# Kernel optimization log

Measured on AMD Instinct MI355X. Metric: run time of the kernel, lower is better.

Reference implementation:

```python
import jax, jax.numpy as jnp
import numpy as np

D_MODEL = 1024
H = 16
D_HEAD = 64  # d_q = d_k = d_v
B = 2
S = 2048


def setup_inputs() -> dict:
    key = jax.random.key(0)
    ks = jax.random.split(key, 12)
    scale = 1.0 / np.sqrt(D_MODEL)
    inp = {
        "q": jax.random.normal(ks[0], (B, S, D_MODEL), dtype=jnp.float32),
        "k": jax.random.normal(ks[1], (B, S, D_MODEL), dtype=jnp.float32),
        "v": jax.random.normal(ks[2], (B, S, D_MODEL), dtype=jnp.float32),
        "mask": jax.random.uniform(ks[3], (S, S), dtype=jnp.float32),
        # stacked per-head projection weights: [H, d_model, d_head]
        "W_q": jax.random.normal(ks[4], (H, D_MODEL, D_HEAD), dtype=jnp.float32) * scale,
        "b_q": jnp.zeros((H, D_HEAD), dtype=jnp.float32),
        "W_k": jax.random.normal(ks[5], (H, D_MODEL, D_HEAD), dtype=jnp.float32) * scale,
        "b_k": jnp.zeros((H, D_HEAD), dtype=jnp.float32),
        "W_v": jax.random.normal(ks[6], (H, D_MODEL, D_HEAD), dtype=jnp.float32) * scale,
        "b_v": jnp.zeros((H, D_HEAD), dtype=jnp.float32),
        # output projection: [H*d_v, d_model]
        "W_o": jax.random.normal(ks[7], (H * D_HEAD, D_MODEL), dtype=jnp.float32) * (1.0 / np.sqrt(H * D_HEAD)),
        "b_o": jnp.zeros((D_MODEL,), dtype=jnp.float32),
    }
    return inp


def reference(q, k, v, mask, W_q, b_q, W_k, b_k, W_v, b_v, W_o, b_o):
    # Batched QKV projections over all heads (original loops per head).
    Q = jnp.einsum("bsd,hde->bhse", q, W_q) + b_q[None, :, None, :]  # [B,H,S,Dh]
    K = jnp.einsum("bsd,hde->bhse", k, W_k) + b_k[None, :, None, :]
    V = jnp.einsum("bsd,hde->bhse", v, W_v) + b_v[None, :, None, :]
    scale = 1.0 / jnp.sqrt(jnp.asarray(D_HEAD, dtype=Q.dtype))
    # NOTE: mask is MULTIPLICATIVE on the scaled scores (as in the original).
    scores = jnp.einsum("bhse,bhte->bhst", Q, K) * scale * mask  # [B,H,S,S]
    attn = jax.nn.softmax(scores, axis=-1)
    heads = jnp.einsum("bhst,bhte->bhse", attn, V)  # [B,H,S,Dh]
    # concat heads along feature dim (head order matches torch cat order)
    concat = jnp.transpose(heads, (0, 2, 1, 3)).reshape(B, S, H * D_HEAD)
    return concat @ W_o + b_o
```

## Files before the change

### kernel.cpp

```cpp
#include <hip/hip_runtime.h>
#include <stdint.h>

#define DM 1024
#define HNUM 16
#define DH 64
#define BB 2
#define SSEQ 2048

typedef unsigned short ushort_t;
typedef __attribute__((ext_vector_type(8))) short bf16x8;
typedef __attribute__((ext_vector_type(4))) float f32x4;
typedef __attribute__((ext_vector_type(16))) float f32x16;

#define SCALE2 0.18033688011112042f
#define DEFER_THR 11.0f

__device__ __forceinline__ ushort_t f2bf(float f) {
  unsigned u = __builtin_bit_cast(unsigned, f);
  u += 0x7FFFu + ((u >> 16) & 1u);
  return (ushort_t)(u >> 16);
}
__device__ __forceinline__ float bf2f(ushort_t h) {
  return __builtin_bit_cast(float, (unsigned)h << 16);
}
__device__ __forceinline__ float fast_exp2(float x) {
#if __has_builtin(__builtin_amdgcn_exp2f)
  return __builtin_amdgcn_exp2f(x);
#else
  return exp2f(x);
#endif
}
__device__ __forceinline__ unsigned cvt_pk_bf16(float lo, float hi) {
  unsigned r;
  asm("v_cvt_pk_bf16_f32 %0, %1, %2" : "=v"(r) : "v"(lo), "v"(hi));
  return r;
}
__device__ __forceinline__ void plane32_swap(unsigned& a, unsigned& b, int hh) {
#if __has_builtin(__builtin_amdgcn_permlane32_swap)
  typedef int v2i __attribute__((ext_vector_type(2)));
  v2i r = __builtin_amdgcn_permlane32_swap((int)a, (int)b, 0, 0);
  a = (unsigned)r.x; b = (unsigned)r.y;
#else
  unsigned sa = (unsigned)__shfl_xor((int)a, 32);
  unsigned sb = (unsigned)__shfl_xor((int)b, 32);
  unsigned na = hh ? sb : a;
  unsigned nb = hh ? b : sa;
  a = na; b = nb;
#endif
}

typedef const __attribute__((address_space(1))) unsigned int* gas_ptr;
typedef __attribute__((address_space(3))) unsigned int* las_ptr;
__device__ __forceinline__ void gload_lds16(const void* g, void* l) {
  __builtin_amdgcn_global_load_lds((gas_ptr)(uintptr_t)g, (las_ptr)(uintptr_t)l, 16, 0, 0);
}

__global__ void cvt_f32_bf16(const float* __restrict__ src, ushort_t* __restrict__ dst, int n8) {
  int idx = blockIdx.x * 256 + threadIdx.x;
  if (idx >= n8) return;
  const float4* s4 = (const float4*)src;
  float4 a = s4[idx * 2], c = s4[idx * 2 + 1];
  union { ushort_t h[8]; uint4 u; } o;
  o.h[0] = f2bf(a.x); o.h[1] = f2bf(a.y); o.h[2] = f2bf(a.z); o.h[3] = f2bf(a.w);
  o.h[4] = f2bf(c.x); o.h[5] = f2bf(c.y); o.h[6] = f2bf(c.z); o.h[7] = f2bf(c.w);
  ((uint4*)dst)[idx] = o.u;
}

__global__ void mask_pack(const float* __restrict__ src, ushort_t* __restrict__ dst) {
  const int TG = blockIdx.x;
  const int T = TG >> 6, G = TG & 63;
  const int tid = threadIdx.x;
  #pragma unroll
  for (int i = 0; i < 2; ++i) {
    const int wd = tid * 2 + i;
    const int l = wd & 63, g2 = (wd >> 6) & 3, a = wd >> 8;
    const int q = G * 32 + (l & 31);
    const int t = T * 64 + a * 32 + g2 * 8 + (l >> 5) * 4;
    float4 mv = *(const float4*)(src + (size_t)q * 2048 + t);
    union { ushort_t h4[4]; uint2 u; } pk;
    pk.h4[0] = f2bf(mv.x * SCALE2); pk.h4[1] = f2bf(mv.y * SCALE2);
    pk.h4[2] = f2bf(mv.z * SCALE2); pk.h4[3] = f2bf(mv.w * SCALE2);
    *(uint2*)(dst + (size_t)TG * 2048 + (size_t)wd * 4) = pk.u;
  }
}

__global__ void transpose_cvt(const float* __restrict__ src, ushort_t* __restrict__ dst, int R, int C) {
  __shared__ ushort_t T[64][65];
  const int g = blockIdx.z;
  const int r0 = blockIdx.y * 64, c0 = blockIdx.x * 64;
  src += (size_t)g * R * C;
  dst += (size_t)g * R * C;
  const int tid = threadIdx.x;
  #pragma unroll
  for (int i = 0; i < 16; ++i) {
    int idx = i * 256 + tid;
    int r = idx >> 6, c = idx & 63;
    T[r][c] = f2bf(src[(size_t)(r0 + r) * C + c0 + c]);
  }
  __syncthreads();
  #pragma unroll
  for (int i = 0; i < 16; ++i) {
    int idx = i * 256 + tid;
    int cc = idx >> 6, rr = idx & 63;
    dst[(size_t)(c0 + cc) * R + r0 + rr] = T[rr][cc];
  }
}

__device__ __forceinline__ void gemm_mainloop_128(const ushort_t* __restrict__ A,
                                                  const ushort_t* __restrict__ Bm,
                                                  f32x4 (&acc)[4][4], int m0, int n0, int l, int w) {
  __shared__ ushort_t As[128 * 64];
  __shared__ ushort_t Bs[128 * 64];
  const int wr = w >> 1, wc = w & 1;
  for (int ks = 0; ks < 16; ++ks) {
    const int k0 = ks * 64;
    #pragma unroll
    for (int it = 0; it < 4; ++it) {
      const int chunk = it * 4 + w;
      const int row = chunk * 8 + (l >> 3);
      const int kc = ((l & 7) * 8) ^ ((row & 7) * 8);
      gload_lds16(A + (size_t)(m0 + row) * 1024 + k0 + kc, (char*)As + chunk * 1024);
      gload_lds16(Bm + (size_t)(n0 + row) * 1024 + k0 + kc, (char*)Bs + chunk * 1024);
    }
    __syncthreads();
    #pragma unroll
    for (int kk = 0; kk < 2; ++kk) {
      bf16x8 af[4], bfr[4];
      #pragma unroll
      for (int mi = 0; mi < 4; ++mi) {
        const int row = wr * 64 + mi * 16 + (l & 15);
        const int kc = (kk * 32 + (l >> 4) * 8) ^ ((row & 7) * 8);
        af[mi] = *(const bf16x8*)(As + row * 64 + kc);
      }
      #pragma unroll
      for (int ni = 0; ni < 4; ++ni) {
        const int row = wc * 64 + ni * 16 + (l & 15);
        const int kc = (kk * 32 + (l >> 4) * 8) ^ ((row & 7) * 8);
        bfr[ni] = *(const bf16x8*)(Bs + row * 64 + kc);
      }
      #pragma unroll
      for (int mi = 0; mi < 4; ++mi)
        #pragma unroll
        for (int ni = 0; ni < 4; ++ni)
          acc[mi][ni] = __builtin_amdgcn_mfma_f32_16x16x32_bf16(af[mi], bfr[ni], acc[mi][ni], 0, 0, 0);
    }
    __syncthreads();
  }
}

__global__ __launch_bounds__(256, 2) void qkv_gemm(
    const ushort_t* __restrict__ qb, const ushort_t* __restrict__ kb, const ushort_t* __restrict__ vb,
    const ushort_t* __restrict__ Wtq, const ushort_t* __restrict__ Wtk, const ushort_t* __restrict__ Wtv,
    const float* __restrict__ bq, const float* __restrict__ bk, const float* __restrict__ bv,
    ushort_t* __restrict__ Qo, ushort_t* __restrict__ Ko, ushort_t* __restrict__ Vto) {
  const int z = blockIdx.z;
  const ushort_t* A  = z == 0 ? qb : (z == 1 ? kb : vb);
  const ushort_t* Bm = z == 0 ? Wtq : (z == 1 ? Wtk : Wtv);
  const float* bias  = z == 0 ? bq : (z == 1 ? bk : bv);
  ushort_t* out      = z == 0 ? Qo : (z == 1 ? Ko : Vto);
  const int m0 = blockIdx.x * 128, n0 = blockIdx.y * 128;
  const int tid = threadIdx.x, l = tid & 63, w = tid >> 6;
  f32x4 acc[4][4] = {};
  gemm_mainloop_128(A, Bm, acc, m0, n0, l, w);
  const int wr = w >> 1, wc = w & 1;
  #pragma unroll
  for (int mi = 0; mi < 4; ++mi) {
    #pragma unroll
    for (int ni = 0; ni < 4; ++ni) {
      const int n = n0 + wc * 64 + ni * 16 + (l & 15);
      const float bb = bias[n];
      const int mbase = m0 + wr * 64 + mi * 16 + ((l >> 4) << 2);
      if (z < 2) {
        #pragma unroll
        for (int i = 0; i < 4; ++i) {
          const int m = mbase + i;
          const size_t o = (((size_t)((m >> 11) * 16 + (n >> 6))) * 2048 + (m & 2047)) * 64 + (n & 63);
          out[o] = f2bf(acc[mi][ni][i] + bb);
        }
      } else {
        union { ushort_t h[4]; uint2 u2; } pk;
        #pragma unroll
        for (int i = 0; i < 4; ++i) pk.h[i] = f2bf(acc[mi][ni][i] + bb);
        const size_t o = (((size_t)((mbase >> 11) * 16 + (n >> 6))) * 64 + (n & 63)) * 2048 + (mbase & 2047);
        *(uint2*)(out + o) = pk.u2;
      }
    }
  }
}

__global__ __launch_bounds__(256, 2) void out_gemm(const ushort_t* __restrict__ A,
                                                   const ushort_t* __restrict__ Bm,
                                                   const float* __restrict__ bias,
                                                   float* __restrict__ out) {
  const int m0 = blockIdx.x * 128, n0 = blockIdx.y * 128;
  const int tid = threadIdx.x, l = tid & 63, w = tid >> 6;
  f32x4 acc[4][4] = {};
  gemm_mainloop_128(A, Bm, acc, m0, n0, l, w);
  const int wr = w >> 1, wc = w & 1;
  #pragma unroll
  for (int mi = 0; mi < 4; ++mi) {
    #pragma unroll
    for (int ni = 0; ni < 4; ++ni) {
      const int n = n0 + wc * 64 + ni * 16 + (l & 15);
      const float bb = bias[n];
      const int mbase = m0 + wr * 64 + mi * 16 + ((l >> 4) << 2);
      #pragma unroll
      for (int i = 0; i < 4; ++i)
        out[(size_t)(mbase + i) * 1024 + n] = acc[mi][ni][i] + bb;
    }
  }
}

__device__ __forceinline__ void stage_kv(const ushort_t* __restrict__ Kb, const ushort_t* __restrict__ Vb,
                                         int t0, ushort_t* ks, ushort_t* vs, int l, int w) {
  #pragma unroll
  for (int half = 0; half < 2; ++half) {
    const int c = half * 4 + w;
    const int r1 = c * 8 + (l >> 3);
    const int cc = ((l & 7) * 8) ^ ((r1 & 7) * 8);
    gload_lds16(Kb + (size_t)(t0 + r1) * 64 + cc, (char*)ks + c * 1024);
    gload_lds16(Vb + (size_t)r1 * 2048 + t0 + cc, (char*)vs + c * 1024);
  }
}

__global__ __launch_bounds__(256, 2) void flash_attn(const ushort_t* __restrict__ Q,
                                                     const ushort_t* __restrict__ K,
                                                     const ushort_t* __restrict__ Vt,
                                                     const ushort_t* __restrict__ maskF,
                                                     ushort_t* __restrict__ concat) {
  const int bh = blockIdx.y, b = bh >> 4, h = bh & 15;
  const int tid = threadIdx.x, l = tid & 63, w = tid >> 6;
  const int hh = l >> 5, q_l = l & 31;
  __shared__ ushort_t Ks[2][64 * 64];
  __shared__ ushort_t Vs[2][64 * 64];
  const ushort_t* Qb = Q + (size_t)bh * 2048 * 64;
  const ushort_t* Kb = K + (size_t)bh * 2048 * 64;
  const ushort_t* Vb = Vt + (size_t)bh * 64 * 2048;
  const int qbase = blockIdx.x * 128 + w * 32;
  const int G = qbase >> 5;

  bf16x8 qf[4];
  #pragma unroll
  for (int s = 0; s < 4; ++s)
    qf[s] = *(const bf16x8*)(Qb + (size_t)(qbase + q_l) * 64 + s * 16 + hh * 8);

  float m_run = -1e30f, l_run = 0.f;
  f32x16 po[2] = {};

  stage_kv(Kb, Vb, 0, Ks[0], Vs[0], l, w);
  int cur = 0;

  for (int t0 = 0; t0 < 2048; t0 += 64) {
    __syncthreads();
    if (t0 + 64 < 2048) stage_kv(Kb, Vb, t0 + 64, Ks[cur ^ 1], Vs[cur ^ 1], l, w);

    const ushort_t* mbase = maskF + (size_t)((t0 >> 6) * 64 + G) * 2048;
    uint2 mw[2][4];
    #pragma unroll
    for (int a = 0; a < 2; ++a)
      #pragma unroll
      for (int g2 = 0; g2 < 4; ++g2)
        mw[a][g2] = *(const uint2*)(mbase + (size_t)(((a * 4 + g2) * 64) + l) * 4);

    f32x16 sc[2] = {};
    #pragma unroll
    for (int s = 0; s < 4; ++s) {
      #pragma unroll
      for (int mt = 0; mt < 2; ++mt) {
        const int row = mt * 32 + q_l;
        const int col = (s * 16 + hh * 8) ^ ((row & 7) * 8);
        const bf16x8 kf = *(const bf16x8*)(Ks[cur] + row * 64 + col);
        sc[mt] = __builtin_amdgcn_mfma_f32_32x32x16_bf16(kf, qf[s], sc[mt], 0, 0, 0);
      }
    }

    float tmax = -1e30f;
    #pragma unroll
    for (int a = 0; a < 2; ++a) {
      #pragma unroll
      for (int g2 = 0; g2 < 4; ++g2) {
        const unsigned lo = mw[a][g2].x, hi = mw[a][g2].y;
        float v0 = sc[a][g2 * 4 + 0] * bf2f((ushort_t)lo);
        float v1 = sc[a][g2 * 4 + 1] * bf2f((ushort_t)(lo >> 16));
        float v2 = sc[a][g2 * 4 + 2] * bf2f((ushort_t)hi);
        float v3 = sc[a][g2 * 4 + 3] * bf2f((ushort_t)(hi >> 16));
        sc[a][g2 * 4 + 0] = v0; sc[a][g2 * 4 + 1] = v1;
        sc[a][g2 * 4 + 2] = v2; sc[a][g2 * 4 + 3] = v3;
        tmax = fmaxf(tmax, fmaxf(fmaxf(v0, v1), fmaxf(v2, v3)));
      }
    }
    tmax = fmaxf(tmax, __shfl_xor(tmax, 32));

    if (!__all(tmax <= m_run + DEFER_THR)) {
      const float mnew = fmaxf(m_run, tmax);
      const float rf = fast_exp2(m_run - mnew);
      m_run = mnew;
      l_run *= rf;
      #pragma unroll
      for (int et = 0; et < 2; ++et)
        #pragma unroll
        for (int r = 0; r < 16; ++r) po[et][r] *= rf;
    }

    float psum = 0.f;
    unsigned pw[2][8];
    #pragma unroll
    for (int a = 0; a < 2; ++a)
      #pragma unroll
      for (int j = 0; j < 8; ++j) {
        const float p0 = fast_exp2(sc[a][2 * j] - m_run);
        const float p1 = fast_exp2(sc[a][2 * j + 1] - m_run);
        psum += p0 + p1;
        pw[a][j] = cvt_pk_bf16(p0, p1);
      }
    psum += __shfl_xor(psum, 32);
    l_run += psum;

    #pragma unroll
    for (int a = 0; a < 2; ++a) {
      plane32_swap(pw[a][0], pw[a][2], hh);
      plane32_swap(pw[a][1], pw[a][3], hh);
      plane32_swap(pw[a][4], pw[a][6], hh);
      plane32_swap(pw[a][5], pw[a][7], hh);
    }

    #pragma unroll
    for (int s = 0; s < 4; ++s) {
      union { unsigned u[4]; bf16x8 v; } pf;
      pf.u[0] = pw[s >> 1][(s & 1) * 4 + 0];
      pf.u[1] = pw[s >> 1][(s & 1) * 4 + 1];
      pf.u[2] = pw[s >> 1][(s & 1) * 4 + 2];
      pf.u[3] = pw[s >> 1][(s & 1) * 4 + 3];
      #pragma unroll
      for (int et = 0; et < 2; ++et) {
        const int row = et * 32 + q_l;
        const int col = (s * 16 + hh * 8) ^ ((row & 7) * 8);
        const bf16x8 vf = *(const bf16x8*)(Vs[cur] + row * 64 + col);
        po[et] = __builtin_amdgcn_mfma_f32_32x32x16_bf16(vf, pf.v, po[et], 0, 0, 0);
      }
    }
    cur ^= 1;
  }

  const float invl = 1.0f / l_run;
  __syncthreads();
  ushort_t* ow = &Ks[0][0] + w * 2048;
  #pragma unroll
  for (int et = 0; et < 2; ++et)
    #pragma unroll
    for (int r = 0; r < 16; ++r) {
      const int e = et * 32 + (r & 3) + 8 * (r >> 2) + 4 * hh;
      const int ba = (q_l * 128 + e * 2) ^ ((q_l & 7) << 4);
      *(ushort_t*)((char*)ow + ba) = f2bf(po[et][r] * invl);
    }
  __syncthreads();
  {
    union { ushort_t hs[32]; uint2 u2[8]; uint4 u4[4]; } ov;
    const int ebase = hh * 32;
    #pragma unroll
    for (int c = 0; c < 8; ++c) {
      const int e0 = ebase + c * 4;
      const int ba = (q_l * 128 + e0 * 2) ^ ((q_l & 7) << 4);
      ov.u2[c] = *(const uint2*)((const char*)ow + ba);
    }
    ushort_t* dst = concat + ((size_t)(b * 2048 + qbase + q_l)) * 1024 + h * 64 + ebase;
    #pragma unroll
    for (int c2 = 0; c2 < 4; ++c2)
      ((uint4*)dst)[c2] = ov.u4[c2];
  }
}

extern "C" void kernel_launch(void* const* d_in, const int* in_sizes, int n_in,
                              void* d_out, int out_size, void* d_ws, size_t ws_size,
                              hipStream_t stream) {
  const float* q    = (const float*)d_in[0];
  const float* k    = (const float*)d_in[1];
  const float* v    = (const float*)d_in[2];
  const float* mask = (const float*)d_in[3];
  const float* Wq   = (const float*)d_in[4];
  const float* bq   = (const float*)d_in[5];
  const float* Wk   = (const float*)d_in[6];
  const float* bk   = (const float*)d_in[7];
  const float* Wv   = (const float*)d_in[8];
  const float* bv   = (const float*)d_in[9];
  const float* Wo   = (const float*)d_in[10];
  const float* bo   = (const float*)d_in[11];

  const size_t SZ8M = (size_t)4096 * 1024 * 2;
  const size_t SZ2M = (size_t)1024 * 1024 * 2;
  if (ws_size < 7 * SZ8M + 4 * SZ2M) return;

  char* p = (char*)d_ws;
  ushort_t* qb    = (ushort_t*)p; p += SZ8M;
  ushort_t* kb    = (ushort_t*)p; p += SZ8M;
  ushort_t* vb    = (ushort_t*)p; p += SZ8M;
  ushort_t* maskb = (ushort_t*)p; p += SZ8M;
  ushort_t* Qo    = (ushort_t*)p; p += SZ8M;
  ushort_t* Ko    = (ushort_t*)p; p += SZ8M;
  ushort_t* Vto   = (ushort_t*)p; p += SZ8M;
  ushort_t* Wtq   = (ushort_t*)p; p += SZ2M;
  ushort_t* Wtk   = (ushort_t*)p; p += SZ2M;
  ushort_t* Wtv   = (ushort_t*)p; p += SZ2M;
  ushort_t* Wot   = (ushort_t*)p; p += SZ2M;
  ushort_t* concat = qb;

  const int n8 = (4096 * 1024) / 8;
  cvt_f32_bf16<<<dim3(2048), dim3(256), 0, stream>>>(q, qb, n8);
  cvt_f32_bf16<<<dim3(2048), dim3(256), 0, stream>>>(k, kb, n8);
  cvt_f32_bf16<<<dim3(2048), dim3(256), 0, stream>>>(v, vb, n8);
  mask_pack<<<dim3(2048), dim3(256), 0, stream>>>(mask, maskb);
  transpose_cvt<<<dim3(1, 16, 16), dim3(256), 0, stream>>>(Wq, Wtq, 1024, 64);
  transpose_cvt<<<dim3(1, 16, 16), dim3(256), 0, stream>>>(Wk, Wtk, 1024, 64);
  transpose_cvt<<<dim3(1, 16, 16), dim3(256), 0, stream>>>(Wv, Wtv, 1024, 64);
  transpose_cvt<<<dim3(16, 16, 1), dim3(256), 0, stream>>>(Wo, Wot, 1024, 1024);
  qkv_gemm<<<dim3(32, 8, 3), dim3(256), 0, stream>>>(qb, kb, vb, Wtq, Wtk, Wtv, bq, bk, bv, Qo, Ko, Vto);
  flash_attn<<<dim3(16, 32), dim3(256), 0, stream>>>(Qo, Ko, Vto, maskb, concat);
  out_gemm<<<dim3(32, 8), dim3(256), 0, stream>>>(concat, Wot, bo, (float*)d_out);
}
```

Before: 151.8 us.

## Widen attention KV tile, retile output GEMM, fuse prep launches

The flash attention loop now stages 128-key K/V tiles per barrier and processes them as two 64-key sub-tiles, which halves the number of syncs. It also raises wave priority around the MFMA blocks and swaps the cross-half shuffles for permlane32 swaps. The output GEMM moves to 64x128 tiles with its own LDS-staged loop, doubling the grid for better CU occupancy. The q/k/v conversions and the three weight transposes are each merged into a single launch to cut launch overhead. In exchange, the attention kernel uses twice the LDS, which may reduce occupancy.

```diff
diff --git a/kernel.cpp b/kernel.cpp
--- a/kernel.cpp
+++ b/kernel.cpp
@@ -48,6 +48,16 @@
   a = na; b = nb;
 #endif
 }
+__device__ __forceinline__ float xhalf_max(float x, int hh) {
+  unsigned a = __builtin_bit_cast(unsigned, x), b = a;
+  plane32_swap(a, b, hh);
+  return fmaxf(__builtin_bit_cast(float, a), __builtin_bit_cast(float, b));
+}
+__device__ __forceinline__ float xhalf_sum(float x, int hh) {
+  unsigned a = __builtin_bit_cast(unsigned, x), b = a;
+  plane32_swap(a, b, hh);
+  return __builtin_bit_cast(float, a) + __builtin_bit_cast(float, b);
+}
 
 typedef const __attribute__((address_space(1))) unsigned int* gas_ptr;
 typedef __attribute__((address_space(3))) unsigned int* las_ptr;
@@ -55,9 +65,14 @@
   __builtin_amdgcn_global_load_lds((gas_ptr)(uintptr_t)g, (las_ptr)(uintptr_t)l, 16, 0, 0);
 }
 
-__global__ void cvt_f32_bf16(const float* __restrict__ src, ushort_t* __restrict__ dst, int n8) {
-  int idx = blockIdx.x * 256 + threadIdx.x;
-  if (idx >= n8) return;
+__global__ void cvt3_f32_bf16(const float* __restrict__ q, const float* __restrict__ k,
+                              const float* __restrict__ v,
+                              ushort_t* __restrict__ qd, ushort_t* __restrict__ kd,
+                              ushort_t* __restrict__ vd) {
+  const int z = blockIdx.y;
+  const float* src = z == 0 ? q : (z == 1 ? k : v);
+  ushort_t* dst    = z == 0 ? qd : (z == 1 ? kd : vd);
+  const int idx = blockIdx.x * 256 + threadIdx.x;
   const float4* s4 = (const float4*)src;
   float4 a = s4[idx * 2], c = s4[idx * 2 + 1];
   union { ushort_t h[8]; uint4 u; } o;
@@ -84,12 +99,34 @@
   }
 }
 
+__global__ void transpose_cvt3(const float* __restrict__ Wq, const float* __restrict__ Wk,
+                               const float* __restrict__ Wv,
+                               ushort_t* __restrict__ dq, ushort_t* __restrict__ dk,
+                               ushort_t* __restrict__ dv) {
+  __shared__ ushort_t T[64][65];
+  const int mat = blockIdx.z >> 4, g = blockIdx.z & 15;
+  const float* src = (mat == 0 ? Wq : (mat == 1 ? Wk : Wv)) + (size_t)g * 1024 * 64;
+  ushort_t* dst    = (mat == 0 ? dq : (mat == 1 ? dk : dv)) + (size_t)g * 1024 * 64;
+  const int r0 = blockIdx.y * 64;
+  const int tid = threadIdx.x;
+  #pragma unroll
+  for (int i = 0; i < 16; ++i) {
+    int idx = i * 256 + tid;
+    int r = idx >> 6, c = idx & 63;
+    T[r][c] = f2bf(src[(size_t)(r0 + r) * 64 + c]);
+  }
+  __syncthreads();
+  #pragma unroll
+  for (int i = 0; i < 16; ++i) {
+    int idx = i * 256 + tid;
+    int cc = idx >> 6, rr = idx & 63;
+    dst[(size_t)cc * 1024 + r0 + rr] = T[rr][cc];
+  }
+}
+
 __global__ void transpose_cvt(const float* __restrict__ src, ushort_t* __restrict__ dst, int R, int C) {
   __shared__ ushort_t T[64][65];
-  const int g = blockIdx.z;
   const int r0 = blockIdx.y * 64, c0 = blockIdx.x * 64;
-  src += (size_t)g * R * C;
-  dst += (size_t)g * R * C;
   const int tid = threadIdx.x;
   #pragma unroll
   for (int i = 0; i < 16; ++i) {
@@ -192,18 +229,59 @@
                                                    const ushort_t* __restrict__ Bm,
                                                    const float* __restrict__ bias,
                                                    float* __restrict__ out) {
-  const int m0 = blockIdx.x * 128, n0 = blockIdx.y * 128;
+  __shared__ ushort_t As[64 * 64];
+  __shared__ ushort_t Bs[128 * 64];
+  const int m0 = blockIdx.x * 64, n0 = blockIdx.y * 128;
   const int tid = threadIdx.x, l = tid & 63, w = tid >> 6;
-  f32x4 acc[4][4] = {};
-  gemm_mainloop_128(A, Bm, acc, m0, n0, l, w);
   const int wr = w >> 1, wc = w & 1;
-  #pragma unroll
-  for (int mi = 0; mi < 4; ++mi) {
+  f32x4 acc[2][4] = {};
+  for (int ks = 0; ks < 16; ++ks) {
+    const int k0 = ks * 64;
+    #pragma unroll
+    for (int it = 0; it < 6; ++it) {
+      const int chunk = it * 4 + w;
+      if (chunk < 8) {
+        const int row = chunk * 8 + (l >> 3);
+        const int kc = ((l & 7) * 8) ^ ((row & 7) * 8);
+        gload_lds16(A + (size_t)(m0 + row) * 1024 + k0 + kc, (char*)As + chunk * 1024);
+      } else {
+        const int c2 = chunk - 8;
+        const int row = c2 * 8 + (l >> 3);
+        const int kc = ((l & 7) * 8) ^ ((row & 7) * 8);
+        gload_lds16(Bm + (size_t)(n0 + row) * 1024 + k0 + kc, (char*)Bs + c2 * 1024);
+      }
+    }
+    __syncthreads();
+    #pragma unroll
+    for (int kk = 0; kk < 2; ++kk) {
+      bf16x8 af[2], bfr[4];
+      #pragma unroll
+      for (int mi = 0; mi < 2; ++mi) {
+        const int row = wr * 32 + mi * 16 + (l & 15);
+        const int kc = (kk * 32 + (l >> 4) * 8) ^ ((row & 7) * 8);
+        af[mi] = *(const bf16x8*)(As + row * 64 + kc);
+      }
+      #pragma unroll
+      for (int ni = 0; ni < 4; ++ni) {
+        const int row = wc * 64 + ni * 16 + (l & 15);
+        const int kc = (kk * 32 + (l >> 4) * 8) ^ ((row & 7) * 8);
+        bfr[ni] = *(const bf16x8*)(Bs + row * 64 + kc);
+      }
+      #pragma unroll
+      for (int mi = 0; mi < 2; ++mi)
+        #pragma unroll
+        for (int ni = 0; ni < 4; ++ni)
+          acc[mi][ni] = __builtin_amdgcn_mfma_f32_16x16x32_bf16(af[mi], bfr[ni], acc[mi][ni], 0, 0, 0);
+    }
+    __syncthreads();
+  }
+  #pragma unroll
+  for (int mi = 0; mi < 2; ++mi) {
     #pragma unroll
     for (int ni = 0; ni < 4; ++ni) {
       const int n = n0 + wc * 64 + ni * 16 + (l & 15);
       const float bb = bias[n];
-      const int mbase = m0 + wr * 64 + mi * 16 + ((l >> 4) << 2);
+      const int mbase = m0 + wr * 32 + mi * 16 + ((l >> 4) << 2);
       #pragma unroll
       for (int i = 0; i < 4; ++i)
         out[(size_t)(mbase + i) * 1024 + n] = acc[mi][ni][i] + bb;
@@ -211,14 +289,20 @@
   }
 }
 
-__device__ __forceinline__ void stage_kv(const ushort_t* __restrict__ Kb, const ushort_t* __restrict__ Vb,
-                                         int t0, ushort_t* ks, ushort_t* vs, int l, int w) {
-  #pragma unroll
-  for (int half = 0; half < 2; ++half) {
-    const int c = half * 4 + w;
+__device__ __forceinline__ void stage_kv128(const ushort_t* __restrict__ Kb, const ushort_t* __restrict__ Vb,
+                                            int t0, ushort_t* ks, ushort_t* vs, int l, int w) {
+  #pragma unroll
+  for (int i = 0; i < 4; ++i) {
+    const int c = i * 4 + w;
     const int r1 = c * 8 + (l >> 3);
     const int cc = ((l & 7) * 8) ^ ((r1 & 7) * 8);
     gload_lds16(Kb + (size_t)(t0 + r1) * 64 + cc, (char*)ks + c * 1024);
+  }
+  #pragma unroll
+  for (int i = 0; i < 4; ++i) {
+    const int c = i * 4 + w;
+    const int r1 = c * 4 + (l >> 4);
+    const int cc = ((l & 15) * 8) ^ ((r1 & 7) * 8);
     gload_lds16(Vb + (size_t)r1 * 2048 + t0 + cc, (char*)vs + c * 1024);
   }
 }
@@ -231,8 +315,8 @@
   const int bh = blockIdx.y, b = bh >> 4, h = bh & 15;
   const int tid = threadIdx.x, l = tid & 63, w = tid >> 6;
   const int hh = l >> 5, q_l = l & 31;
-  __shared__ ushort_t Ks[2][64 * 64];
-  __shared__ ushort_t Vs[2][64 * 64];
+  __shared__ ushort_t Ks[2][128 * 64];
+  __shared__ ushort_t Vs[2][64 * 128];
   const ushort_t* Qb = Q + (size_t)bh * 2048 * 64;
   const ushort_t* Kb = K + (size_t)bh * 2048 * 64;
   const ushort_t* Vb = Vt + (size_t)bh * 64 * 2048;
@@ -247,97 +331,103 @@
   float m_run = -1e30f, l_run = 0.f;
   f32x16 po[2] = {};
 
-  stage_kv(Kb, Vb, 0, Ks[0], Vs[0], l, w);
+  stage_kv128(Kb, Vb, 0, Ks[0], Vs[0], l, w);
   int cur = 0;
 
-  for (int t0 = 0; t0 < 2048; t0 += 64) {
+  for (int t0 = 0; t0 < 2048; t0 += 128) {
     __syncthreads();
-    if (t0 + 64 < 2048) stage_kv(Kb, Vb, t0 + 64, Ks[cur ^ 1], Vs[cur ^ 1], l, w);
-
-    const ushort_t* mbase = maskF + (size_t)((t0 >> 6) * 64 + G) * 2048;
-    uint2 mw[2][4];
-    #pragma unroll
-    for (int a = 0; a < 2; ++a)
-      #pragma unroll
-      for (int g2 = 0; g2 < 4; ++g2)
-        mw[a][g2] = *(const uint2*)(mbase + (size_t)(((a * 4 + g2) * 64) + l) * 4);
-
-    f32x16 sc[2] = {};
-    #pragma unroll
-    for (int s = 0; s < 4; ++s) {
-      #pragma unroll
-      for (int mt = 0; mt < 2; ++mt) {
-        const int row = mt * 32 + q_l;
-        const int col = (s * 16 + hh * 8) ^ ((row & 7) * 8);
-        const bf16x8 kf = *(const bf16x8*)(Ks[cur] + row * 64 + col);
-        sc[mt] = __builtin_amdgcn_mfma_f32_32x32x16_bf16(kf, qf[s], sc[mt], 0, 0, 0);
-      }
-    }
-
-    float tmax = -1e30f;
-    #pragma unroll
-    for (int a = 0; a < 2; ++a) {
-      #pragma unroll
-      for (int g2 = 0; g2 < 4; ++g2) {
-        const unsigned lo = mw[a][g2].x, hi = mw[a][g2].y;
-        float v0 = sc[a][g2 * 4 + 0] * bf2f((ushort_t)lo);
-        float v1 = sc[a][g2 * 4 + 1] * bf2f((ushort_t)(lo >> 16));
-        float v2 = sc[a][g2 * 4 + 2] * bf2f((ushort_t)hi);
-        float v3 = sc[a][g2 * 4 + 3] * bf2f((ushort_t)(hi >> 16));
-        sc[a][g2 * 4 + 0] = v0; sc[a][g2 * 4 + 1] = v1;
-        sc[a][g2 * 4 + 2] = v2; sc[a][g2 * 4 + 3] = v3;
-        tmax = fmaxf(tmax, fmaxf(fmaxf(v0, v1), fmaxf(v2, v3)));
-      }
-    }
-    tmax = fmaxf(tmax, __shfl_xor(tmax, 32));
-
-    if (!__all(tmax <= m_run + DEFER_THR)) {
-      const float mnew = fmaxf(m_run, tmax);
-      const float rf = fast_exp2(m_run - mnew);
-      m_run = mnew;
-      l_run *= rf;
-      #pragma unroll
-      for (int et = 0; et < 2; ++et)
-        #pragma unroll
-        for (int r = 0; r < 16; ++r) po[et][r] *= rf;
-    }
-
-    float psum = 0.f;
-    unsigned pw[2][8];
-    #pragma unroll
-    for (int a = 0; a < 2; ++a)
-      #pragma unroll
-      for (int j = 0; j < 8; ++j) {
-        const float p0 = fast_exp2(sc[a][2 * j] - m_run);
-        const float p1 = fast_exp2(sc[a][2 * j + 1] - m_run);
-        psum += p0 + p1;
-        pw[a][j] = cvt_pk_bf16(p0, p1);
-      }
-    psum += __shfl_xor(psum, 32);
-    l_run += psum;
-
-    #pragma unroll
-    for (int a = 0; a < 2; ++a) {
-      plane32_swap(pw[a][0], pw[a][2], hh);
-      plane32_swap(pw[a][1], pw[a][3], hh);
-      plane32_swap(pw[a][4], pw[a][6], hh);
-      plane32_swap(pw[a][5], pw[a][7], hh);
-    }
-
-    #pragma unroll
-    for (int s = 0; s < 4; ++s) {
-      union { unsigned u[4]; bf16x8 v; } pf;
-      pf.u[0] = pw[s >> 1][(s & 1) * 4 + 0];
-      pf.u[1] = pw[s >> 1][(s & 1) * 4 + 1];
-      pf.u[2] = pw[s >> 1][(s & 1) * 4 + 2];
-      pf.u[3] = pw[s >> 1][(s & 1) * 4 + 3];
-      #pragma unroll
-      for (int et = 0; et < 2; ++et) {
-        const int row = et * 32 + q_l;
-        const int col = (s * 16 + hh * 8) ^ ((row & 7) * 8);
-        const bf16x8 vf = *(const bf16x8*)(Vs[cur] + row * 64 + col);
-        po[et] = __builtin_amdgcn_mfma_f32_32x32x16_bf16(vf, pf.v, po[et], 0, 0, 0);
-      }
+    if (t0 + 128 < 2048) stage_kv128(Kb, Vb, t0 + 128, Ks[cur ^ 1], Vs[cur ^ 1], l, w);
+
+    #pragma unroll
+    for (int sub = 0; sub < 2; ++sub) {
+      const ushort_t* mbase = maskF + (size_t)(((t0 >> 6) + sub) * 64 + G) * 2048;
+      uint2 mw[2][4];
+      #pragma unroll
+      for (int a = 0; a < 2; ++a)
+        #pragma unroll
+        for (int g2 = 0; g2 < 4; ++g2)
+          mw[a][g2] = *(const uint2*)(mbase + (size_t)(((a * 4 + g2) * 64) + l) * 4);
+
+      f32x16 sc[2] = {};
+      __builtin_amdgcn_s_setprio(1);
+      #pragma unroll
+      for (int s = 0; s < 4; ++s) {
+        #pragma unroll
+        for (int mt = 0; mt < 2; ++mt) {
+          const int row = sub * 64 + mt * 32 + q_l;
+          const int col = (s * 16 + hh * 8) ^ ((q_l & 7) * 8);
+          const bf16x8 kf = *(const bf16x8*)(Ks[cur] + row * 64 + col);
+          sc[mt] = __builtin_amdgcn_mfma_f32_32x32x16_bf16(kf, qf[s], sc[mt], 0, 0, 0);
+        }
+      }
+      __builtin_amdgcn_s_setprio(0);
+
+      float tmax = -1e30f;
+      #pragma unroll
+      for (int a = 0; a < 2; ++a) {
+        #pragma unroll
+        for (int g2 = 0; g2 < 4; ++g2) {
+          const unsigned lo = mw[a][g2].x, hi = mw[a][g2].y;
+          float v0 = sc[a][g2 * 4 + 0] * bf2f((ushort_t)lo);
+          float v1 = sc[a][g2 * 4 + 1] * bf2f((ushort_t)(lo >> 16));
+          float v2 = sc[a][g2 * 4 + 2] * bf2f((ushort_t)hi);
+          float v3 = sc[a][g2 * 4 + 3] * bf2f((ushort_t)(hi >> 16));
+          sc[a][g2 * 4 + 0] = v0; sc[a][g2 * 4 + 1] = v1;
+          sc[a][g2 * 4 + 2] = v2; sc[a][g2 * 4 + 3] = v3;
+          tmax = fmaxf(tmax, fmaxf(fmaxf(v0, v1), fmaxf(v2, v3)));
+        }
+      }
+      tmax = xhalf_max(tmax, hh);
+
+      if (!__all(tmax <= m_run + DEFER_THR)) {
+        const float mnew = fmaxf(m_run, tmax);
+        const float rf = fast_exp2(m_run - mnew);
+        m_run = mnew;
+        l_run *= rf;
+        #pragma unroll
+        for (int et = 0; et < 2; ++et)
+          #pragma unroll
+          for (int r = 0; r < 16; ++r) po[et][r] *= rf;
+      }
+
+      float psum = 0.f;
+      unsigned pw[2][8];
+      #pragma unroll
+      for (int a = 0; a < 2; ++a)
+        #pragma unroll
+        for (int j = 0; j < 8; ++j) {
+          const float p0 = fast_exp2(sc[a][2 * j] - m_run);
+          const float p1 = fast_exp2(sc[a][2 * j + 1] - m_run);
+          psum += p0 + p1;
+          pw[a][j] = cvt_pk_bf16(p0, p1);
+        }
+      l_run += xhalf_sum(psum, hh);
+
+      #pragma unroll
+      for (int a = 0; a < 2; ++a) {
+        plane32_swap(pw[a][0], pw[a][2], hh);
+        plane32_swap(pw[a][1], pw[a][3], hh);
+        plane32_swap(pw[a][4], pw[a][6], hh);
+        plane32_swap(pw[a][5], pw[a][7], hh);
+      }
+
+      __builtin_amdgcn_s_setprio(1);
+      #pragma unroll
+      for (int s = 0; s < 4; ++s) {
+        union { unsigned u[4]; bf16x8 v; } pf;
+        pf.u[0] = pw[s >> 1][(s & 1) * 4 + 0];
+        pf.u[1] = pw[s >> 1][(s & 1) * 4 + 1];
+        pf.u[2] = pw[s >> 1][(s & 1) * 4 + 2];
+        pf.u[3] = pw[s >> 1][(s & 1) * 4 + 3];
+        #pragma unroll
+        for (int et = 0; et < 2; ++et) {
+          const int row = et * 32 + q_l;
+          const int col = sub * 64 + ((s * 16 + hh * 8) ^ ((q_l & 7) * 8));
+          const bf16x8 vf = *(const bf16x8*)(Vs[cur] + row * 128 + col);
+          po[et] = __builtin_amdgcn_mfma_f32_32x32x16_bf16(vf, pf.v, po[et], 0, 0, 0);
+        }
+      }
+      __builtin_amdgcn_s_setprio(0);
     }
     cur ^= 1;
   }
@@ -404,16 +494,11 @@
   ushort_t* Wot   = (ushort_t*)p; p += SZ2M;
   ushort_t* concat = qb;
 
-  const int n8 = (4096 * 1024) / 8;
-  cvt_f32_bf16<<<dim3(2048), dim3(256), 0, stream>>>(q, qb, n8);
-  cvt_f32_bf16<<<dim3(2048), dim3(256), 0, stream>>>(k, kb, n8);
-  cvt_f32_bf16<<<dim3(2048), dim3(256), 0, stream>>>(v, vb, n8);
+  cvt3_f32_bf16<<<dim3(2048, 3), dim3(256), 0, stream>>>(q, k, v, qb, kb, vb);
   mask_pack<<<dim3(2048), dim3(256), 0, stream>>>(mask, maskb);
-  transpose_cvt<<<dim3(1, 16, 16), dim3(256), 0, stream>>>(Wq, Wtq, 1024, 64);
-  transpose_cvt<<<dim3(1, 16, 16), dim3(256), 0, stream>>>(Wk, Wtk, 1024, 64);
-  transpose_cvt<<<dim3(1, 16, 16), dim3(256), 0, stream>>>(Wv, Wtv, 1024, 64);
-  transpose_cvt<<<dim3(16, 16, 1), dim3(256), 0, stream>>>(Wo, Wot, 1024, 1024);
+  transpose_cvt3<<<dim3(1, 16, 48), dim3(256), 0, stream>>>(Wq, Wk, Wv, Wtq, Wtk, Wtv);
+  transpose_cvt<<<dim3(16, 16), dim3(256), 0, stream>>>(Wo, Wot, 1024, 1024);
   qkv_gemm<<<dim3(32, 8, 3), dim3(256), 0, stream>>>(qb, kb, vb, Wtq, Wtk, Wtv, bq, bk, bv, Qo, Ko, Vto);
   flash_attn<<<dim3(16, 32), dim3(256), 0, stream>>>(Qo, Ko, Vto, maskb, concat);
-  out_gemm<<<dim3(32, 8), dim3(256), 0, stream>>>(concat, Wot, bo, (float*)d_out);
-}
+  out_gemm<<<dim3(64, 8), dim3(256), 0, stream>>>(concat, Wot, bo, (float*)d_out);
+}
```

Result: faster. 144.7 us (-4.6%).
